# Optimization experiments

Measured on AMD Instinct MI355X. Metric: run time of the kernel, lower is better.

Reference implementation:

```python
import jax, jax.numpy as jnp
import numpy as np

N_SRC = 50000
N_DST = 50000
E = 800000
D = 64


def setup_inputs() -> dict:
    key = jax.random.key(0)
    k1, k2, k3, k4 = jax.random.split(key, 4)
    src_emb = jax.random.normal(k1, (N_SRC, D), dtype=jnp.float32)
    e_att = jax.random.uniform(k2, (E, 1), dtype=jnp.float32)
    src_idx = jax.random.randint(k3, (E,), 0, N_SRC, dtype=jnp.int64)
    dst_idx = jax.random.randint(k4, (E,), 0, N_DST, dtype=jnp.int64)
    return {"src_emb": src_emb, "e_att": e_att, "src_idx": src_idx, "dst_idx": dst_idx}


def reference(src_emb, e_att, src_idx, dst_idx):
    # DGL: fn.src_mul_edge('emb_o','att','msg') then fn.sum('msg','emb_n')
    # msg[e] = src_emb[src_idx[e]] * e_att[e]  -> scatter-sum into dst nodes
    msg = src_emb[src_idx] * e_att                      # [E, D]
    emb_n = jax.ops.segment_sum(msg, dst_idx, num_segments=N_DST)  # [N_DST, D]
    return emb_n
```

## Files before the change

kernel.cpp:

```cpp
#include <hip/hip_runtime.h>
#include <hip/hip_fp16.h>


#define D 64
#define CAP 64
#define OVF_CAP 65536
#define NPART 8

__global__ void __launch_bounds__(256)
scatter_conv_kernel(const int* __restrict__ dst_idx, const int* __restrict__ src_idx,
                    const float* __restrict__ e_att, int* __restrict__ cursor,
                    unsigned* __restrict__ payload,
                    int* __restrict__ ovf_count, int* __restrict__ ovf_list,
                    const float* __restrict__ src_emb, __half* __restrict__ emb_h,
                    int E, int n_dst, int rpx, int epb4, int SB, int n4) {
    if ((int)blockIdx.x >= SB) {
        int i = ((int)blockIdx.x - SB) * 256 + threadIdx.x;
        if (i < n4) {
            float4 v = ((const float4*)src_emb)[i];
            ushort4 h;
            h.x = __half_as_ushort(__float2half(v.x));
            h.y = __half_as_ushort(__float2half(v.y));
            h.z = __half_as_ushort(__float2half(v.z));
            h.w = __half_as_ushort(__float2half(v.w));
            ((ushort4*)emb_h)[i] = h;
        }
        return;
    }

    int x     = blockIdx.x & (NPART - 1);
    int chunk = blockIdx.x >> 3;
    int lo  = x * rpx;
    int hi  = min(lo + rpx, n_dst);
    unsigned span = (unsigned)(hi - lo);

    int E4 = E >> 2;
    int i0 = chunk * epb4;
    int i1 = min(i0 + epb4, E4);

    for (int i = i0 + threadIdx.x; i < i1; i += 256) {
        int4 d4 = ((const int4*)dst_idx)[i];
        bool m0 = (unsigned)(d4.x - lo) < span;
        bool m1 = (unsigned)(d4.y - lo) < span;
        bool m2 = (unsigned)(d4.z - lo) < span;
        bool m3 = (unsigned)(d4.w - lo) < span;
        if (!(m0 | m1 | m2 | m3)) continue;
        int4   s4 = ((const int4*)src_idx)[i];
        float4 a4 = ((const float4*)e_att)[i];
        int   dd[4] = {d4.x, d4.y, d4.z, d4.w};
        int   ss[4] = {s4.x, s4.y, s4.z, s4.w};
        float aa[4] = {a4.x, a4.y, a4.z, a4.w};
        bool  mm[4] = {m0, m1, m2, m3};
#pragma unroll
        for (int k = 0; k < 4; ++k) {
            if (!mm[k]) continue;
            int d = dd[k];
            int p = atomicAdd(&cursor[d], 1);
            unsigned pay = (unsigned)ss[k] |
                           ((unsigned)__half_as_ushort(__float2half(aa[k])) << 16);
            if (p < CAP) {
                payload[(size_t)d * CAP + p] = pay;
            } else {
                int oi = atomicAdd(ovf_count, 1);
                if (oi < OVF_CAP) ovf_list[oi] = 4 * i + k;
            }
        }
    }
    if (chunk == 0) {
        for (int e = (E4 << 2) + threadIdx.x; e < E; e += 256) {
            int d = dst_idx[e];
            if ((unsigned)(d - lo) >= span) continue;
            int p = atomicAdd(&cursor[d], 1);
            unsigned pay = (unsigned)src_idx[e] |
                           ((unsigned)__half_as_ushort(__float2half(e_att[e])) << 16);
            if (p < CAP) payload[(size_t)d * CAP + p] = pay;
            else { int oi = atomicAdd(ovf_count, 1); if (oi < OVF_CAP) ovf_list[oi] = e; }
        }
    }
}

__global__ void __launch_bounds__(256)
gather2_kernel(const __half* __restrict__ emb_h,
               const unsigned* __restrict__ payload,
               const int* __restrict__ cursor,
               const int* __restrict__ dst_idx, const int* __restrict__ src_idx,
               const float* __restrict__ e_att, const float* __restrict__ src_emb,
               const int* __restrict__ ovf_count, const int* __restrict__ ovf_list,
               float* __restrict__ out, int n_dst, int n_src, int rpx) {
    int x    = blockIdx.x & (NPART - 1);
    int g    = blockIdx.x >> 3;
    int wv   = threadIdx.x >> 6;
    int lane = threadIdx.x & 63;
    int sub  = lane >> 5;
    int l31  = lane & 31;

    int local = (g * 4 + wv) * 2 + sub;
    int w = x * rpx + local;
    bool rowvalid = (local < rpx) && (w < n_dst);

    int cn  = rowvalid ? cursor[w] : 0;
    int cnt = min(cn, CAP);
    int c32 = min(cnt, 32);

    unsigned pp = 0u;
    if (rowvalid) pp = payload[(size_t)w * CAP + l31];

    int cmax = max(c32, __shfl_xor(c32, 32));

    float2 acc = make_float2(0.f, 0.f);
    unsigned smax = (unsigned)(n_src - 1);
    for (int j = 0; j < cmax; j += 4) {
        int sl = (sub << 5) + j;
        unsigned pv0 = (unsigned)__shfl((int)pp, sl);
        unsigned pv1 = (unsigned)__shfl((int)pp, sl + 1);
        unsigned pv2 = (unsigned)__shfl((int)pp, sl + 2);
        unsigned pv3 = (unsigned)__shfl((int)pp, sl + 3);
        float a0 = (j     < c32) ? __half2float(__ushort_as_half((unsigned short)(pv0 >> 16))) : 0.f;
        float a1 = (j + 1 < c32) ? __half2float(__ushort_as_half((unsigned short)(pv1 >> 16))) : 0.f;
        float a2 = (j + 2 < c32) ? __half2float(__ushort_as_half((unsigned short)(pv2 >> 16))) : 0.f;
        float a3 = (j + 3 < c32) ? __half2float(__ushort_as_half((unsigned short)(pv3 >> 16))) : 0.f;
        unsigned s0 = min(pv0 & 0xffffu, smax);
        unsigned s1 = min(pv1 & 0xffffu, smax);
        unsigned s2 = min(pv2 & 0xffffu, smax);
        unsigned s3 = min(pv3 & 0xffffu, smax);
        __half2 h0 = ((const __half2*)(emb_h + (size_t)s0 * D))[l31];
        __half2 h1 = ((const __half2*)(emb_h + (size_t)s1 * D))[l31];
        __half2 h2 = ((const __half2*)(emb_h + (size_t)s2 * D))[l31];
        __half2 h3 = ((const __half2*)(emb_h + (size_t)s3 * D))[l31];
        acc.x = fmaf(__low2float(h0),  a0, acc.x);
        acc.y = fmaf(__high2float(h0), a0, acc.y);
        acc.x = fmaf(__low2float(h1),  a1, acc.x);
        acc.y = fmaf(__high2float(h1), a1, acc.y);
        acc.x = fmaf(__low2float(h2),  a2, acc.x);
        acc.y = fmaf(__high2float(h2), a2, acc.y);
        acc.x = fmaf(__low2float(h3),  a3, acc.x);
        acc.y = fmaf(__high2float(h3), a3, acc.y);
    }

    if (rowvalid & (cnt > 32)) {
        for (int j = 32; j < cnt; ++j) {
            unsigned pv = payload[(size_t)w * CAP + j];
            float a = __half2float(__ushort_as_half((unsigned short)(pv >> 16)));
            unsigned s = min(pv & 0xffffu, smax);
            __half2 h = ((const __half2*)(emb_h + (size_t)s * D))[l31];
            acc.x = fmaf(__low2float(h),  a, acc.x);
            acc.y = fmaf(__high2float(h), a, acc.y);
        }
    }

    if (rowvalid) {
        if (cn > CAP) {
            int oc = *ovf_count;
            if (oc > OVF_CAP) oc = OVF_CAP;
            for (int i = 0; i < oc; ++i) {
                int e = ovf_list[i];
                if (dst_idx[e] == w) {
                    float a = e_att[e];
                    int   s = src_idx[e];
                    acc.x = fmaf(src_emb[(size_t)s * D + 2 * l31],     a, acc.x);
                    acc.y = fmaf(src_emb[(size_t)s * D + 2 * l31 + 1], a, acc.y);
                }
            }
        }
        ((float2*)(out + (size_t)w * D))[l31] = acc;
    }
}

__global__ void __launch_bounds__(256)
atomic_fallback_kernel(const float* __restrict__ src_emb, const float* __restrict__ e_att,
                       const int* __restrict__ src_idx, const int* __restrict__ dst_idx,
                       float* __restrict__ out, int E) {
    int tid  = blockIdx.x * blockDim.x + threadIdx.x;
    int e    = tid >> 4;
    int part = tid & 15;
    if (e >= E) return;
    int   s = src_idx[e];
    int   d = dst_idx[e];
    float a = e_att[e];
    float4 v = ((const float4*)src_emb)[(size_t)s * 16 + part];
    float* orow = out + (size_t)d * D + part * 4;
    atomicAdd(orow + 0, v.x * a);
    atomicAdd(orow + 1, v.y * a);
    atomicAdd(orow + 2, v.z * a);
    atomicAdd(orow + 3, v.w * a);
}

extern "C" void kernel_launch(void* const* d_in, const int* in_sizes, int n_in,
                              void* d_out, int out_size, void* d_ws, size_t ws_size,
                              hipStream_t stream) {
    const float* src_emb = (const float*)d_in[0];
    const float* e_att   = (const float*)d_in[1];
    const int*   src_idx = (const int*)d_in[2];
    const int*   dst_idx = (const int*)d_in[3];
    float*       out     = (float*)d_out;

    const int E     = in_sizes[2];
    const int n_dst = out_size / D;
    const int n_src = in_sizes[0] / D;

    size_t off_emb = 0;
    size_t off_pay = off_emb + (size_t)n_src * D / 2;
    size_t off_cur = off_pay + (size_t)n_dst * CAP;
    size_t need_ints = off_cur + (size_t)n_dst + 1 + OVF_CAP;

    if (n_src <= 65536 && ws_size >= need_ints * sizeof(int)) {
        __half*   emb_h   = (__half*)d_ws;
        unsigned* payload = (unsigned*)d_ws + off_pay;
        int*      cursor  = (int*)d_ws + off_cur;
        int*      ovf_count = cursor + n_dst;
        int*      ovf_list  = ovf_count + 1;

        hipMemsetAsync(cursor, 0, ((size_t)n_dst + 1) * sizeof(int), stream);

        const int rpx = (n_dst + NPART - 1) / NPART;
        const int chunks = 512;
        const int SB = chunks * NPART;
        const int E4 = E >> 2;
        const int epb4 = (E4 + chunks - 1) / chunks;
        const int n4 = n_src * D / 4;
        const int CB = (n4 + 255) / 256;

        scatter_conv_kernel<<<SB + CB, 256, 0, stream>>>(
            dst_idx, src_idx, e_att, cursor, payload, ovf_count, ovf_list,
            src_emb, emb_h, E, n_dst, rpx, epb4, SB, n4);

        const int gpb = (rpx + 7) / 8;
        gather2_kernel<<<gpb * NPART, 256, 0, stream>>>(
            emb_h, payload, cursor, dst_idx, src_idx, e_att, src_emb,
            ovf_count, ovf_list, out, n_dst, n_src, rpx);
        return;
    }

    hipMemsetAsync(d_out, 0, (size_t)out_size * sizeof(float), stream);
    atomic_fallback_kernel<<<(E * 16 + 255) / 256, 256, 0, stream>>>(
        src_emb, e_att, src_idx, dst_idx, out, E);
}
```

Measured before the change: 131.1 us.

## Fuse memset, scatter and gather into one cooperative kernel with grid syncs

Replaces the memset plus two-kernel pipeline with a single cooperative kernel of 1024 blocks. It zeroes cursors and converts embeddings to half, grid-syncs, bucket-scatters edges by destination, grid-syncs again, then gathers with a grid-stride loop over row groups. The gather inner loop is widened from 4 to 8 loads in flight. This removes launch and memset overhead but adds two grid-wide barriers and a fixed grid size. If the cooperative launch fails, the code falls back to the old path.

```diff
diff --git a/kernel.cpp b/kernel.cpp
--- a/kernel.cpp
+++ b/kernel.cpp
@@ -1,11 +1,171 @@
 #include <hip/hip_runtime.h>
 #include <hip/hip_fp16.h>
+#include <hip/hip_cooperative_groups.h>
+
+namespace cg = cooperative_groups;
 
 
 #define D 64
 #define CAP 64
 #define OVF_CAP 65536
 #define NPART 8
+#define FGRID 1024
+#define FCHUNKS (FGRID / NPART)
+
+__global__ void __launch_bounds__(256, 4)
+fused_kernel(const int* __restrict__ dst_idx, const int* __restrict__ src_idx,
+             const float* __restrict__ e_att, int* __restrict__ cursor,
+             unsigned* __restrict__ payload,
+             int* __restrict__ ovf_count, int* __restrict__ ovf_list,
+             const float* __restrict__ src_emb, __half* __restrict__ emb_h,
+             float* __restrict__ out,
+             int E, int n_dst, int n_src, int rpx, int epb4, int n4) {
+    const int tid  = threadIdx.x;
+    const int gtid = (int)blockIdx.x * 256 + tid;
+    const int nthr = FGRID * 256;
+
+    for (int i = gtid; i < n_dst + 1; i += nthr) cursor[i] = 0;
+    for (int i = gtid; i < n4; i += nthr) {
+        float4 v = ((const float4*)src_emb)[i];
+        ushort4 h;
+        h.x = __half_as_ushort(__float2half(v.x));
+        h.y = __half_as_ushort(__float2half(v.y));
+        h.z = __half_as_ushort(__float2half(v.z));
+        h.w = __half_as_ushort(__float2half(v.w));
+        ((ushort4*)emb_h)[i] = h;
+    }
+    cg::this_grid().sync();
+
+    const int x     = blockIdx.x & (NPART - 1);
+    const int chunk = (int)blockIdx.x >> 3;
+    {
+        int lo = x * rpx;
+        int hi = min(lo + rpx, n_dst);
+        unsigned span = (unsigned)(hi - lo);
+        int E4 = E >> 2;
+        int i0 = chunk * epb4;
+        int i1 = min(i0 + epb4, E4);
+
+        for (int i = i0 + tid; i < i1; i += 256) {
+            int4 d4 = ((const int4*)dst_idx)[i];
+            bool m0 = (unsigned)(d4.x - lo) < span;
+            bool m1 = (unsigned)(d4.y - lo) < span;
+            bool m2 = (unsigned)(d4.z - lo) < span;
+            bool m3 = (unsigned)(d4.w - lo) < span;
+            if (!(m0 | m1 | m2 | m3)) continue;
+            int4   s4 = ((const int4*)src_idx)[i];
+            float4 a4 = ((const float4*)e_att)[i];
+            int   dd[4] = {d4.x, d4.y, d4.z, d4.w};
+            int   ss[4] = {s4.x, s4.y, s4.z, s4.w};
+            float aa[4] = {a4.x, a4.y, a4.z, a4.w};
+            bool  mm[4] = {m0, m1, m2, m3};
+#pragma unroll
+            for (int k = 0; k < 4; ++k) {
+                if (!mm[k]) continue;
+                int d = dd[k];
+                int p = atomicAdd(&cursor[d], 1);
+                unsigned pay = (unsigned)ss[k] |
+                               ((unsigned)__half_as_ushort(__float2half(aa[k])) << 16);
+                if (p < CAP) {
+                    payload[(size_t)d * CAP + p] = pay;
+                } else {
+                    int oi = atomicAdd(ovf_count, 1);
+                    if (oi < OVF_CAP) ovf_list[oi] = 4 * i + k;
+                }
+            }
+        }
+        if (chunk == 0) {
+            for (int e = (E4 << 2) + tid; e < E; e += 256) {
+                int d = dst_idx[e];
+                if ((unsigned)(d - lo) >= span) continue;
+                int p = atomicAdd(&cursor[d], 1);
+                unsigned pay = (unsigned)src_idx[e] |
+                               ((unsigned)__half_as_ushort(__float2half(e_att[e])) << 16);
+                if (p < CAP) payload[(size_t)d * CAP + p] = pay;
+                else { int oi = atomicAdd(ovf_count, 1); if (oi < OVF_CAP) ovf_list[oi] = e; }
+            }
+        }
+    }
+    cg::this_grid().sync();
+
+    {
+        int wv   = tid >> 6;
+        int lane = tid & 63;
+        int sub  = lane >> 5;
+        int l31  = lane & 31;
+        int ngroups = (rpx + 7) / 8;
+        unsigned smax = (unsigned)(n_src - 1);
+
+        for (int g = chunk; g < ngroups; g += FCHUNKS) {
+            int local = (g * 4 + wv) * 2 + sub;
+            int w = x * rpx + local;
+            bool rowvalid = (local < rpx) && (w < n_dst);
+
+            int cn  = rowvalid ? cursor[w] : 0;
+            int cnt = min(cn, CAP);
+            int c32 = min(cnt, 32);
+
+            unsigned pp = 0u;
+            if (rowvalid) pp = payload[(size_t)w * CAP + l31];
+
+            int cmax = max(c32, __shfl_xor(c32, 32));
+
+            float2 acc = make_float2(0.f, 0.f);
+            for (int j = 0; j < cmax; j += 8) {
+                unsigned pv[8];
+                float    aw[8];
+                unsigned sidx[8];
+#pragma unroll
+                for (int k = 0; k < 8; ++k)
+                    pv[k] = (unsigned)__shfl((int)pp, (sub << 5) + j + k);
+#pragma unroll
+                for (int k = 0; k < 8; ++k) {
+                    aw[k] = (j + k < c32)
+                          ? __half2float(__ushort_as_half((unsigned short)(pv[k] >> 16)))
+                          : 0.f;
+                    sidx[k] = min(pv[k] & 0xffffu, smax);
+                }
+                __half2 h[8];
+#pragma unroll
+                for (int k = 0; k < 8; ++k)
+                    h[k] = ((const __half2*)(emb_h + (size_t)sidx[k] * D))[l31];
+#pragma unroll
+                for (int k = 0; k < 8; ++k) {
+                    acc.x = fmaf(__low2float(h[k]),  aw[k], acc.x);
+                    acc.y = fmaf(__high2float(h[k]), aw[k], acc.y);
+                }
+            }
+
+            if (rowvalid & (cnt > 32)) {
+                for (int j = 32; j < cnt; ++j) {
+                    unsigned pv = payload[(size_t)w * CAP + j];
+                    float a = __half2float(__ushort_as_half((unsigned short)(pv >> 16)));
+                    unsigned s = min(pv & 0xffffu, smax);
+                    __half2 hh = ((const __half2*)(emb_h + (size_t)s * D))[l31];
+                    acc.x = fmaf(__low2float(hh),  a, acc.x);
+                    acc.y = fmaf(__high2float(hh), a, acc.y);
+                }
+            }
+
+            if (rowvalid) {
+                if (cn > CAP) {
+                    int oc = *ovf_count;
+                    if (oc > OVF_CAP) oc = OVF_CAP;
+                    for (int i = 0; i < oc; ++i) {
+                        int e = ovf_list[i];
+                        if (dst_idx[e] == w) {
+                            float a = e_att[e];
+                            int   s = src_idx[e];
+                            acc.x = fmaf(src_emb[(size_t)s * D + 2 * l31],     a, acc.x);
+                            acc.y = fmaf(src_emb[(size_t)s * D + 2 * l31 + 1], a, acc.y);
+                        }
+                    }
+                }
+                ((float2*)(out + (size_t)w * D))[l31] = acc;
+            }
+        }
+    }
+}
 
 __global__ void __launch_bounds__(256)
 scatter_conv_kernel(const int* __restrict__ dst_idx, const int* __restrict__ src_idx,
@@ -27,17 +187,14 @@
         }
         return;
     }
-
     int x     = blockIdx.x & (NPART - 1);
     int chunk = blockIdx.x >> 3;
     int lo  = x * rpx;
     int hi  = min(lo + rpx, n_dst);
     unsigned span = (unsigned)(hi - lo);
-
     int E4 = E >> 2;
     int i0 = chunk * epb4;
     int i1 = min(i0 + epb4, E4);
-
     for (int i = i0 + threadIdx.x; i < i1; i += 256) {
         int4 d4 = ((const int4*)dst_idx)[i];
         bool m0 = (unsigned)(d4.x - lo) < span;
@@ -58,12 +215,8 @@
             int p = atomicAdd(&cursor[d], 1);
             unsigned pay = (unsigned)ss[k] |
                            ((unsigned)__half_as_ushort(__float2half(aa[k])) << 16);
-            if (p < CAP) {
-                payload[(size_t)d * CAP + p] = pay;
-            } else {
-                int oi = atomicAdd(ovf_count, 1);
-                if (oi < OVF_CAP) ovf_list[oi] = 4 * i + k;
-            }
+            if (p < CAP) payload[(size_t)d * CAP + p] = pay;
+            else { int oi = atomicAdd(ovf_count, 1); if (oi < OVF_CAP) ovf_list[oi] = 4 * i + k; }
         }
     }
     if (chunk == 0) {
@@ -93,20 +246,15 @@
     int lane = threadIdx.x & 63;
     int sub  = lane >> 5;
     int l31  = lane & 31;
-
     int local = (g * 4 + wv) * 2 + sub;
     int w = x * rpx + local;
     bool rowvalid = (local < rpx) && (w < n_dst);
-
     int cn  = rowvalid ? cursor[w] : 0;
     int cnt = min(cn, CAP);
     int c32 = min(cnt, 32);
-
     unsigned pp = 0u;
     if (rowvalid) pp = payload[(size_t)w * CAP + l31];
-
     int cmax = max(c32, __shfl_xor(c32, 32));
-
     float2 acc = make_float2(0.f, 0.f);
     unsigned smax = (unsigned)(n_src - 1);
     for (int j = 0; j < cmax; j += 4) {
@@ -136,7 +284,6 @@
         acc.x = fmaf(__low2float(h3),  a3, acc.x);
         acc.y = fmaf(__high2float(h3), a3, acc.y);
     }
-
     if (rowvalid & (cnt > 32)) {
         for (int j = 32; j < cnt; ++j) {
             unsigned pv = payload[(size_t)w * CAP + j];
@@ -147,7 +294,6 @@
             acc.y = fmaf(__high2float(h), a, acc.y);
         }
     }
-
     if (rowvalid) {
         if (cn > CAP) {
             int oc = *ovf_count;
@@ -210,20 +356,35 @@
         int*      ovf_count = cursor + n_dst;
         int*      ovf_list  = ovf_count + 1;
 
+        int rpx  = (n_dst + NPART - 1) / NPART;
+        int E4   = E >> 2;
+        int epb4 = (E4 + FCHUNKS - 1) / FCHUNKS;
+        int n4   = n_src * D / 4;
+
+        {
+            const int* a_dst = dst_idx; const int* a_src = src_idx;
+            const float* a_att = e_att; const float* a_emb = src_emb;
+            int Ev = E, ndv = n_dst, nsv = n_src, rpxv = rpx, epb4v = epb4, n4v = n4;
+            void* args[] = { (void*)&a_dst, (void*)&a_src, (void*)&a_att,
+                             (void*)&cursor, (void*)&payload,
+                             (void*)&ovf_count, (void*)&ovf_list,
+                             (void*)&a_emb, (void*)&emb_h, (void*)&out,
+                             (void*)&Ev, (void*)&ndv, (void*)&nsv,
+                             (void*)&rpxv, (void*)&epb4v, (void*)&n4v };
+            hipError_t err = hipLaunchCooperativeKernel(
+                (void*)fused_kernel, dim3(FGRID), dim3(256), args, 0, stream);
+            if (err == hipSuccess) return;
+            (void)hipGetLastError();
+        }
+
         hipMemsetAsync(cursor, 0, ((size_t)n_dst + 1) * sizeof(int), stream);
-
-        const int rpx = (n_dst + NPART - 1) / NPART;
         const int chunks = 512;
         const int SB = chunks * NPART;
-        const int E4 = E >> 2;
-        const int epb4 = (E4 + chunks - 1) / chunks;
-        const int n4 = n_src * D / 4;
+        const int epb4f = (E4 + chunks - 1) / chunks;
         const int CB = (n4 + 255) / 256;
-
         scatter_conv_kernel<<<SB + CB, 256, 0, stream>>>(
             dst_idx, src_idx, e_att, cursor, payload, ovf_count, ovf_list,
-            src_emb, emb_h, E, n_dst, rpx, epb4, SB, n4);
-
+            src_emb, emb_h, E, n_dst, rpx, epb4f, SB, n4);
         const int gpb = (rpx + 7) / 8;
         gather2_kernel<<<gpb * NPART, 256, 0, stream>>>(
             emb_h, payload, cursor, dst_idx, src_idx, e_att, src_emb,
```

Measured after the change: 314.9 us. 140% more time.
